# Optimization experiments

Measured on AMD Instinct MI355X. Metric: run time of the kernel, lower is better.

## Reference

```python
import jax, jax.numpy as jnp
import numpy as np

N = 100000
E = 1600000
IN_DIM = 128
OUT_DIM = 128


def setup_inputs() -> dict:
    key = jax.random.key(0)
    k1, k2, k3, k4 = jax.random.split(key, 4)
    x = jax.random.normal(k1, (N, IN_DIM), dtype=jnp.float32)
    edge_index = jax.random.randint(k2, (2, E), 0, N, dtype=jnp.int64)
    # GCNConv linear weight [in, out] and bias [out]
    W = jax.random.normal(k3, (IN_DIM, OUT_DIM), dtype=jnp.float32) / np.sqrt(IN_DIM)
    b = jax.random.normal(k4, (OUT_DIM,), dtype=jnp.float32) * 0.01
    return {"x": x, "edge_index": edge_index, "W": W, "b": b}


def reference(x, edge_index, W, b):
    n = x.shape[0]
    # linear transform first (PyG GCNConv applies lin before propagate)
    h = x @ W  # [N, OUT_DIM]
    # add self-loops
    loops = jnp.arange(n, dtype=edge_index.dtype)
    src = jnp.concatenate([edge_index[0], loops])
    dst = jnp.concatenate([edge_index[1], loops])
    # symmetric degree normalization (degree counted on dst, incl. self-loops)
    deg = jnp.zeros((n,), dtype=h.dtype).at[dst].add(1.0)
    dinv = jnp.where(deg > 0, jax.lax.rsqrt(deg), 0.0)
    norm = dinv[src] * dinv[dst]  # [E+N]
    # gather, scale, scatter-sum
    msgs = h[src] * norm[:, None]  # [E+N, OUT_DIM]
    out = jax.ops.segment_sum(msgs, dst, num_segments=n) + b
    return jax.nn.relu(out)
```

## Files before the change

### kernel.cpp

```cpp
#include <hip/hip_runtime.h>
#include <cstdint>
#include <cstddef>

#define IN_DIM 128
#define OUT_DIM 128
#define NR 8
#define ACAP 448
#define NS 256
#define NSUB_MAX 64
#define LCAP 192
#define SBCAP 4864
#define SCAP 4864

typedef int vint4 __attribute__((ext_vector_type(4)));
typedef float vfloat2 __attribute__((ext_vector_type(2)));
typedef short bf16x8 __attribute__((ext_vector_type(8)));
typedef float f32x4 __attribute__((ext_vector_type(4)));

__device__ __forceinline__ unsigned short f2bf(float f) {
  unsigned int u = __float_as_uint(f);
  u = (u + 0x7FFFu + ((u >> 16) & 1u)) >> 16;
  return (unsigned short)u;
}
__device__ __forceinline__ float bf_lo(unsigned int v) { return __uint_as_float(v << 16); }
__device__ __forceinline__ float bf_hi(unsigned int v) { return __uint_as_float(v & 0xFFFF0000u); }

__global__ void k_zero_i32(int* __restrict__ p, int n) {
  int i = blockIdx.x * blockDim.x + threadIdx.x;
  int st = gridDim.x * blockDim.x;
  for (; i < n; i += st) p[i] = 0;
}

__global__ void k_zero_f32(float* __restrict__ p, long long n) {
  long long i = (long long)blockIdx.x * blockDim.x + threadIdx.x;
  long long st = (long long)gridDim.x * blockDim.x;
  for (; i < n; i += st) p[i] = 0.0f;
}

__global__ void k_init(int* __restrict__ bmeta, int* __restrict__ sbcnt, int nB,
                       const float* __restrict__ W, unsigned short* __restrict__ Wt_g) {
  int gid = blockIdx.x * blockDim.x + threadIdx.x;
  int st = gridDim.x * blockDim.x;
  if (blockIdx.x == 0 && threadIdx.x < 16) bmeta[threadIdx.x] = 0;
  for (int i = gid; i < nB; i += st) sbcnt[i] = 0;
  for (int i = gid; i < IN_DIM * OUT_DIM; i += st) {
    int k = i >> 7, c = i & 127;
    Wt_g[c * IN_DIM + k] = f2bf(W[i]);
  }
}

__global__ void k_hist(const int* __restrict__ dst, int E, int* __restrict__ deg) {
  int i = blockIdx.x * blockDim.x + threadIdx.x;
  int st = gridDim.x * blockDim.x;
  for (; i < E; i += st) atomicAdd(&deg[dst[i]], 1);
}

__global__ void k_dinv(const int* __restrict__ deg, float* __restrict__ dinv, int n) {
  int i = blockIdx.x * blockDim.x + threadIdx.x;
  int st = gridDim.x * blockDim.x;
  for (; i < n; i += st) dinv[i] = rsqrtf((float)(deg[i] + 1));
}

__global__ __launch_bounds__(256) void k_bucket2(const int* __restrict__ ei, int E, int n,
                                                 unsigned int* __restrict__ bkt, int bcap,
                                                 int* __restrict__ bcnt,
                                                 int2* __restrict__ ovf, int* __restrict__ ocnt) {
  __shared__ unsigned int buf[NR][ACAP];
  __shared__ int cnt[NR];
  __shared__ int base[NR];
  const int rs = (n + NR - 1) / NR;
  const int tid = threadIdx.x;
  const int E4 = E >> 2;
  const vint4* s4 = (const vint4*)ei;
  const vint4* d4 = (const vint4*)(ei + E);
  const int nChunks = (E4 + 511) >> 9;

  for (int c = blockIdx.x; c < nChunks; c += gridDim.x) {
    if (tid < NR) cnt[tid] = 0;
    __syncthreads();
    const int i0 = c << 9;
#pragma unroll
    for (int u = 0; u < 2; ++u) {
      int i = i0 + (u << 8) + tid;
      if (i < E4) {
        vint4 s = __builtin_nontemporal_load(&s4[i]);
        vint4 d = __builtin_nontemporal_load(&d4[i]);
#define PUT(dd, ss)                                                                         \
        {                                                                                   \
          int rr = (dd) / rs;                                                               \
          unsigned int w = ((unsigned int)((dd) - rr * rs) << 17) | (unsigned int)(ss);     \
          int pos = atomicAdd(&cnt[rr], 1);                                                 \
          if (pos < ACAP) buf[rr][pos] = w;                                                 \
          else { int op = atomicAdd(ocnt, 1); ovf[op] = make_int2((ss), (dd)); }            \
        }
        PUT(d.x, s.x) PUT(d.y, s.y) PUT(d.z, s.z) PUT(d.w, s.w)
#undef PUT
      }
    }
    __syncthreads();
    if (tid < NR) {
      int m = cnt[tid]; if (m > ACAP) m = ACAP;
      base[tid] = atomicAdd(&bcnt[tid], m);
    }
    __syncthreads();
#pragma unroll
    for (int r = 0; r < NR; ++r) {
      int m = cnt[r]; if (m > ACAP) m = ACAP;
      int b = base[r];
      unsigned int* dp = bkt + (size_t)r * bcap;
      for (int j = tid; j < m; j += 256) {
        int idx = b + j;
        if (idx < bcap) __builtin_nontemporal_store(buf[r][j], &dp[idx]);
        else {
          unsigned int w = buf[r][j];
          int op = atomicAdd(ocnt, 1);
          ovf[op] = make_int2((int)(w & 0x1FFFFu), r * rs + (int)(w >> 17));
        }
      }
    }
    __syncthreads();
  }
  if (blockIdx.x == 0 && tid == 0) {
    for (int i = E4 << 2; i < E; ++i) {
      int s = ei[i], d = ei[E + i];
      int r = d / rs;
      int p = atomicAdd(&bcnt[r], 1);
      if (p < bcap) bkt[(size_t)r * bcap + p] = ((unsigned int)(d - r * rs) << 17) | (unsigned int)s;
      else { int op = atomicAdd(ocnt, 1); ovf[op] = make_int2(s, d); }
    }
  }
}

__global__ __launch_bounds__(256) void k_subbkt(const unsigned int* __restrict__ bkt, int bcap,
                                                const int* __restrict__ bcnt,
                                                unsigned int* __restrict__ sbkt,
                                                int* __restrict__ sbcnt, int nsub, int n,
                                                int2* __restrict__ ovf, int* __restrict__ ocnt) {
  __shared__ unsigned int buf[NSUB_MAX][LCAP];
  __shared__ int cnt[NSUB_MAX];
  __shared__ int base[NSUB_MAX];
  const int tid = threadIdx.x;
  const int r = blockIdx.x & 7;
  const int gblk = blockIdx.x >> 3;
  const int nblk = gridDim.x >> 3;
  const int rs = (n + NR - 1) / NR;
  int cr = bcnt[r]; if (cr > bcap) cr = bcap;
  const unsigned int* bp = bkt + (size_t)r * bcap;
  const int nChunks = (cr + 4095) >> 12;

  for (int c = gblk; c < nChunks; c += nblk) {
    for (int t = tid; t < nsub; t += 256) cnt[t] = 0;
    __syncthreads();
    const int i0 = c << 12;
    const int iend = min(i0 + 4096, cr);
    for (int i = i0 + tid; i < iend; i += 256) {
      unsigned int w = bp[i];
      int sub = (int)(w >> 25);
      int pos = atomicAdd(&cnt[sub], 1);
      if (pos < LCAP) buf[sub][pos] = w;
      else { int op = atomicAdd(ocnt, 1); ovf[op] = make_int2((int)(w & 0x1FFFFu), r * rs + (int)(w >> 17)); }
    }
    __syncthreads();
    for (int t = tid; t < nsub; t += 256) {
      int m = cnt[t]; if (m > LCAP) m = LCAP;
      base[t] = atomicAdd(&sbcnt[t * NR + r], m);
    }
    __syncthreads();
    for (int s = 0; s < nsub; ++s) {
      int m = cnt[s]; if (m > LCAP) m = LCAP;
      int b = base[s];
      unsigned int* dp = sbkt + (size_t)(s * NR + r) * SBCAP;
      for (int j = tid; j < m; j += 256) {
        int idx = b + j;
        if (idx < SBCAP) dp[idx] = buf[s][j];
        else {
          unsigned int w = buf[s][j];
          int op = atomicAdd(ocnt, 1);
          ovf[op] = make_int2((int)(w & 0x1FFFFu), r * rs + (int)(w >> 17));
        }
      }
    }
    __syncthreads();
  }
}

__global__ __launch_bounds__(256) void k_subsort2(const unsigned int* __restrict__ sbkt,
                                                  const int* __restrict__ sbcnt, int n,
                                                  int* __restrict__ csr, int* __restrict__ rs_start,
                                                  int* __restrict__ cur_end, float* __restrict__ dinv) {
  __shared__ unsigned int raw[SBCAP];
  __shared__ unsigned int srt[SBCAP];
  __shared__ int hist[NS];
  __shared__ int pref[NS];
  __shared__ int off[NS];
  const int tid = threadIdx.x;
  const int r = blockIdx.x & 7;
  const int sub = blockIdx.x >> 3;
  const int rs = (n + NR - 1) / NR;
  const int rsz = min(rs, n - r * rs);
  const int lo_dl = sub << 8;
  if (lo_dl >= rsz) return;
  const int nsn = min(NS, rsz - lo_dl);

  hist[tid] = 0;
  __syncthreads();

  int m = sbcnt[blockIdx.x]; if (m > SBCAP) m = SBCAP;
  const unsigned int* bp = sbkt + (size_t)blockIdx.x * SBCAP;
  for (int i = tid; i < m; i += 256) {
    unsigned int w = bp[i];
    raw[i] = w;
    atomicAdd(&hist[(int)(w >> 17) & (NS - 1)], 1);
  }
  __syncthreads();

  pref[tid] = hist[tid];
  __syncthreads();
  for (int o = 1; o < NS; o <<= 1) {
    int v = pref[tid] + ((tid >= o) ? pref[tid - o] : 0);
    __syncthreads();
    pref[tid] = v;
    __syncthreads();
  }
  off[tid] = pref[tid] - hist[tid];
  __syncthreads();

  for (int i = tid; i < m; i += 256) {
    unsigned int w = raw[i];
    int p = atomicAdd(&off[(int)(w >> 17) & (NS - 1)], 1);
    srt[p] = w & 0x1FFFFu;
  }
  __syncthreads();

  const int sbase = blockIdx.x * SCAP;
  for (int i = tid; i < m; i += 256) csr[sbase + i] = (int)srt[i];
  if (tid < nsn) {
    int node = r * rs + lo_dl + tid;
    rs_start[node] = sbase + pref[tid] - hist[tid];
    cur_end[node] = sbase + pref[tid];
    dinv[node] = rsqrtf((float)(hist[tid] + 1));
  }
}

__global__ void k_scatter_ovf(const int2* __restrict__ ovf, const int* __restrict__ ocnt,
                              int* __restrict__ cur_end, int* __restrict__ csr, int csr_total) {
  int m = *ocnt;
  for (int i = blockIdx.x * blockDim.x + threadIdx.x; i < m; i += gridDim.x * blockDim.x) {
    int2 e = ovf[i];
    int p = atomicAdd(&cur_end[e.y], 1);
    if (p >= 0 && p < csr_total) csr[p] = e.x;
  }
}

__global__ __launch_bounds__(256) void k_gemm_mfma(const float* __restrict__ x,
                                                   const unsigned short* __restrict__ Wt_g,
                                                   const float* __restrict__ dinv,
                                                   unsigned short* __restrict__ gb, int M) {
  __shared__ unsigned short xT[64][136];
  __shared__ unsigned short Wt[128][136];
  const int tid = threadIdx.x;
  const int row0 = blockIdx.x * 64;

  for (int i = tid; i < (IN_DIM * OUT_DIM) / 8; i += 256) {
    int c = i >> 4, k8 = (i & 15) * 8;
    uint4 v = *(const uint4*)(Wt_g + (size_t)c * IN_DIM + k8);
    *(uint4*)&Wt[c][k8] = v;
  }
  for (int i = tid; i < (64 * IN_DIM) / 4; i += 256) {
    int idx = i * 4;
    int r = idx >> 7, k = idx & 127;
    int grow = row0 + r; if (grow >= M) grow = M - 1;
    float4 v = *(const float4*)(x + (size_t)grow * IN_DIM + k);
    ushort4 b;
    b.x = f2bf(v.x); b.y = f2bf(v.y); b.z = f2bf(v.z); b.w = f2bf(v.w);
    *(ushort4*)&xT[r][k] = b;
  }
  __syncthreads();

  const int wv = tid >> 6;
  const int lane = tid & 63;
  const int l15 = lane & 15;
  const int lk8 = (lane >> 4) * 8;

  f32x4 acc[8];
#pragma unroll
  for (int ct = 0; ct < 8; ++ct) acc[ct] = (f32x4){0.f, 0.f, 0.f, 0.f};

#pragma unroll
  for (int kt = 0; kt < 4; ++kt) {
    bf16x8 a = *(const bf16x8*)&xT[wv * 16 + l15][kt * 32 + lk8];
#pragma unroll
    for (int ct = 0; ct < 8; ++ct) {
      bf16x8 b = *(const bf16x8*)&Wt[ct * 16 + l15][kt * 32 + lk8];
      acc[ct] = __builtin_amdgcn_mfma_f32_16x16x32_bf16(a, b, acc[ct], 0, 0, 0);
    }
  }

  const int drow0 = wv * 16 + (lane >> 4) * 4;
#pragma unroll
  for (int reg = 0; reg < 4; ++reg) {
    int grow = row0 + drow0 + reg;
    if (grow < M) {
      float s = dinv[grow];
      unsigned short* gp = gb + (size_t)grow * OUT_DIM + l15;
#pragma unroll
      for (int ct = 0; ct < 8; ++ct) {
        gp[ct * 16] = f2bf(acc[ct][reg] * s);
      }
    }
  }
}

__global__ __launch_bounds__(256) void k_gemm_scale(const float* __restrict__ x, const float* __restrict__ W,
                                                    const float* __restrict__ dinv,
                                                    unsigned short* __restrict__ gb, int M) {
  __shared__ float xT[32][128];
  __shared__ float Ws[32][128];
  const int tid = threadIdx.x;
  const int tc = tid & 15;
  const int tr = tid >> 4;
  const int row0 = blockIdx.x * 128;
  const int lr = tid & 127;
  const int lk = (tid >> 7) * 16;

  float acc[8][8] = {};

  for (int k0 = 0; k0 < IN_DIM; k0 += 32) {
    int grow = row0 + lr;
    if (grow >= M) grow = M - 1;
    const float4* xp = (const float4*)(x + (size_t)grow * IN_DIM + k0 + lk);
    float4 a0 = xp[0], a1 = xp[1], a2 = xp[2], a3 = xp[3];
    const float4* wp = (const float4*)(W + (size_t)(k0 + (tid >> 3)) * OUT_DIM + (tid & 7) * 16);
    float4 w0 = wp[0], w1 = wp[1], w2 = wp[2], w3 = wp[3];

    __syncthreads();
    xT[lk + 0][lr] = a0.x;  xT[lk + 1][lr] = a0.y;  xT[lk + 2][lr] = a0.z;  xT[lk + 3][lr] = a0.w;
    xT[lk + 4][lr] = a1.x;  xT[lk + 5][lr] = a1.y;  xT[lk + 6][lr] = a1.z;  xT[lk + 7][lr] = a1.w;
    xT[lk + 8][lr] = a2.x;  xT[lk + 9][lr] = a2.y;  xT[lk + 10][lr] = a2.z; xT[lk + 11][lr] = a2.w;
    xT[lk + 12][lr] = a3.x; xT[lk + 13][lr] = a3.y; xT[lk + 14][lr] = a3.z; xT[lk + 15][lr] = a3.w;
    float4* wsp = (float4*)&Ws[tid >> 3][(tid & 7) * 16];
    wsp[0] = w0; wsp[1] = w1; wsp[2] = w2; wsp[3] = w3;
    __syncthreads();

#pragma unroll
    for (int k = 0; k < 32; ++k) {
      float xv[8], wvv[8];
      *(float4*)&xv[0] = *(const float4*)&xT[k][tr * 8];
      *(float4*)&xv[4] = *(const float4*)&xT[k][tr * 8 + 4];
      *(float4*)&wvv[0] = *(const float4*)&Ws[k][tc * 8];
      *(float4*)&wvv[4] = *(const float4*)&Ws[k][tc * 8 + 4];
#pragma unroll
      for (int ii = 0; ii < 8; ++ii)
#pragma unroll
        for (int jj = 0; jj < 8; ++jj)
          acc[ii][jj] = fmaf(xv[ii], wvv[jj], acc[ii][jj]);
    }
  }

#pragma unroll
  for (int ii = 0; ii < 8; ++ii) {
    int rr = row0 + tr * 8 + ii;
    if (rr < M) {
      float s = dinv[rr];
      uint4 o;
      o.x = (unsigned int)f2bf(acc[ii][0] * s) | ((unsigned int)f2bf(acc[ii][1] * s) << 16);
      o.y = (unsigned int)f2bf(acc[ii][2] * s) | ((unsigned int)f2bf(acc[ii][3] * s) << 16);
      o.z = (unsigned int)f2bf(acc[ii][4] * s) | ((unsigned int)f2bf(acc[ii][5] * s) << 16);
      o.w = (unsigned int)f2bf(acc[ii][6] * s) | ((unsigned int)f2bf(acc[ii][7] * s) << 16);
      *(uint4*)(gb + (size_t)rr * OUT_DIM + tc * 8) = o;
    }
  }
}

__global__ __launch_bounds__(256) void k_agg_se(const unsigned short* __restrict__ gb,
                                                const int* __restrict__ rs_start, const int* __restrict__ cur_end,
                                                const int* __restrict__ csr, const float* __restrict__ dinv,
                                                const float* __restrict__ bias, float* __restrict__ out, int n) {
  const int lane = threadIdx.x & 63;
  const int wave = __builtin_amdgcn_readfirstlane(threadIdx.x >> 6);
  const int wpb = blockDim.x >> 6;
  const int nWaves = gridDim.x * wpb;
  const int c2 = lane * 2;
  const float2 bb = *(const float2*)(bias + c2);

  for (int node = blockIdx.x * wpb + wave; node < n; node += nWaves) {
    const int s = rs_start[node];
    const int e = cur_end[node];
    unsigned int sv = *(const unsigned int*)(gb + (size_t)node * OUT_DIM + c2);
    float ax = bf_lo(sv), ay = bf_hi(sv);
    int i = s;
    for (; i + 8 <= e; i += 8) {
      int s0 = csr[i + 0], s1 = csr[i + 1], s2 = csr[i + 2], s3 = csr[i + 3];
      int s4 = csr[i + 4], s5 = csr[i + 5], s6 = csr[i + 6], s7 = csr[i + 7];
      unsigned int v0 = *(const unsigned int*)(gb + (size_t)s0 * OUT_DIM + c2);
      unsigned int v1 = *(const unsigned int*)(gb + (size_t)s1 * OUT_DIM + c2);
      unsigned int v2 = *(const unsigned int*)(gb + (size_t)s2 * OUT_DIM + c2);
      unsigned int v3 = *(const unsigned int*)(gb + (size_t)s3 * OUT_DIM + c2);
      unsigned int v4 = *(const unsigned int*)(gb + (size_t)s4 * OUT_DIM + c2);
      unsigned int v5 = *(const unsigned int*)(gb + (size_t)s5 * OUT_DIM + c2);
      unsigned int v6 = *(const unsigned int*)(gb + (size_t)s6 * OUT_DIM + c2);
      unsigned int v7 = *(const unsigned int*)(gb + (size_t)s7 * OUT_DIM + c2);
      ax += ((bf_lo(v0) + bf_lo(v1)) + (bf_lo(v2) + bf_lo(v3))) +
            ((bf_lo(v4) + bf_lo(v5)) + (bf_lo(v6) + bf_lo(v7)));
      ay += ((bf_hi(v0) + bf_hi(v1)) + (bf_hi(v2) + bf_hi(v3))) +
            ((bf_hi(v4) + bf_hi(v5)) + (bf_hi(v6) + bf_hi(v7)));
    }
    for (; i < e; ++i) {
      unsigned int v = *(const unsigned int*)(gb + (size_t)csr[i] * OUT_DIM + c2);
      ax += bf_lo(v);
      ay += bf_hi(v);
    }
    const float di = dinv[node];
    vfloat2 o;
    o.x = fmaxf(fmaf(ax, di, bb.x), 0.0f);
    o.y = fmaxf(fmaf(ay, di, bb.y), 0.0f);
    __builtin_nontemporal_store(o, (vfloat2*)(out + (size_t)node * OUT_DIM + c2));
  }
}

__global__ __launch_bounds__(256) void k_scatter(const int* __restrict__ ei, int E,
                                                 const unsigned short* __restrict__ gb, float* __restrict__ out) {
  const int lane = threadIdx.x & 63;
  const int wave = __builtin_amdgcn_readfirstlane(threadIdx.x >> 6);
  const int wpb = blockDim.x >> 6;
  const int nWaves = gridDim.x * wpb;
  const int c2 = lane * 2;
  for (int e = blockIdx.x * wpb + wave; e < E; e += nWaves) {
    int s = ei[e];
    int d = ei[E + e];
    unsigned int v = *(const unsigned int*)(gb + (size_t)s * OUT_DIM + c2);
    atomicAdd(&out[(size_t)d * OUT_DIM + c2 + 0], bf_lo(v));
    atomicAdd(&out[(size_t)d * OUT_DIM + c2 + 1], bf_hi(v));
  }
}

__global__ void k_finalize(const unsigned short* __restrict__ gb, const float* __restrict__ dinv,
                           const float* __restrict__ bias, float* __restrict__ out, int n) {
  int i = blockIdx.x * blockDim.x + threadIdx.x;
  int st = gridDim.x * blockDim.x;
  int total = n * OUT_DIM;
  for (; i < total; i += st) {
    int node = i >> 7;
    float gv = __uint_as_float(((unsigned int)gb[i]) << 16);
    float v = (out[i] + gv) * dinv[node] + bias[i & 127];
    out[i] = fmaxf(v, 0.0f);
  }
}

extern "C" void kernel_launch(void* const* d_in, const int* in_sizes, int n_in,
                              void* d_out, int out_size, void* d_ws, size_t ws_size,
                              hipStream_t stream) {
  const float* x = (const float*)d_in[0];
  const int* ei = (const int*)d_in[1];
  const float* W = (const float*)d_in[2];
  const float* bias = (const float*)d_in[3];
  float* out = (float*)d_out;

  const int N = in_sizes[0] / IN_DIM;
  const int E = in_sizes[1] / 2;

  const int rs = (N + NR - 1) / NR;
  const int nsub = (rs + NS - 1) / NS;
  const int nBlocksB = nsub * NR;
  const int csr_total = nBlocksB * SCAP;
  const int bcap = E / NR + E / 64 + 256;
  const int mBlocks64 = (N + 63) / 64;

  char* ws = (char*)d_ws;
  size_t off = 0;
  auto alloc = [&](size_t bytes) -> void* {
    void* p = ws + off;
    off += (bytes + 255) & ~(size_t)255;
    return p;
  };

  unsigned short* gb = (unsigned short*)alloc((size_t)N * OUT_DIM * sizeof(unsigned short));
  float* dinv = (float*)alloc((size_t)N * sizeof(float));
  int* rs_start = (int*)alloc((size_t)N * sizeof(int));
  int* cur_end = (int*)alloc((size_t)N * sizeof(int));
  int* csr = (int*)alloc((size_t)csr_total * sizeof(int));
  unsigned int* bkt = (unsigned int*)alloc((size_t)NR * bcap * sizeof(unsigned int));
  unsigned int* sbkt = (unsigned int*)alloc((size_t)nBlocksB * SBCAP * sizeof(unsigned int));
  int* sbcnt = (int*)alloc((size_t)nBlocksB * sizeof(int));
  unsigned short* Wt_g = (unsigned short*)alloc((size_t)IN_DIM * OUT_DIM * sizeof(unsigned short));
  int* bmeta = (int*)alloc(16 * sizeof(int));
  int2* ovf = (int2*)alloc((size_t)(E / 8 + 1024) * sizeof(int2));
  size_t bucket_need = off;

  const bool bucketed = (ws_size >= bucket_need) && (N <= (1 << 17)) && (rs <= (1 << 14)) &&
                        (nsub <= NSUB_MAX);

  if (bucketed) {
    k_init<<<64, 256, 0, stream>>>(bmeta, sbcnt, nBlocksB, W, Wt_g);
    int aGrid = ((E >> 2) + 511) >> 9;
    if (aGrid < 1) aGrid = 1;
    k_bucket2<<<aGrid, 256, 0, stream>>>(ei, E, N, bkt, bcap, bmeta, ovf, bmeta + 8);
    k_subbkt<<<nBlocksB, 256, 0, stream>>>(bkt, bcap, bmeta, sbkt, sbcnt, nsub, N, ovf, bmeta + 8);
    k_subsort2<<<nBlocksB, 256, 0, stream>>>(sbkt, sbcnt, N, csr, rs_start, cur_end, dinv);
    k_gemm_mfma<<<mBlocks64, 256, 0, stream>>>(x, Wt_g, dinv, gb, N);
    k_scatter_ovf<<<64, 256, 0, stream>>>(ovf, bmeta + 8, cur_end, csr, csr_total);
    k_agg_se<<<2048, 256, 0, stream>>>(gb, rs_start, cur_end, csr, dinv, bias, out, N);
  } else {
    off = 0;
    unsigned short* gb2 = (unsigned short*)alloc((size_t)N * OUT_DIM * sizeof(unsigned short));
    int* deg = (int*)alloc((size_t)N * sizeof(int));
    float* dinv2 = (float*)alloc((size_t)N * sizeof(float));
    if (ws_size < off) return;
    k_zero_i32<<<256, 256, 0, stream>>>(deg, N);
    k_hist<<<2048, 256, 0, stream>>>(ei + E, E, deg);
    k_dinv<<<512, 256, 0, stream>>>(deg, dinv2, N);
    k_gemm_scale<<<(N + 127) / 128, 256, 0, stream>>>(x, W, dinv2, gb2, N);
    k_zero_f32<<<2048, 256, 0, stream>>>(out, (long long)N * OUT_DIM);
    k_scatter<<<4096, 256, 0, stream>>>(ei, E, gb2, out);
    k_finalize<<<2048, 256, 0, stream>>>(gb2, dinv2, bias, out, N);
  }
}
```

Measured before the change: 152.7 us.

## Split aggregation into two column-half passes to shrink gather working set

```diff
diff --git a/kernel.cpp b/kernel.cpp
--- a/kernel.cpp
+++ b/kernel.cpp
@@ -24,6 +24,7 @@
 }
 __device__ __forceinline__ float bf_lo(unsigned int v) { return __uint_as_float(v << 16); }
 __device__ __forceinline__ float bf_hi(unsigned int v) { return __uint_as_float(v & 0xFFFF0000u); }
+__device__ __forceinline__ float bf1(unsigned short v) { return __uint_as_float(((unsigned int)v) << 16); }
 
 __global__ void k_zero_i32(int* __restrict__ p, int n) {
   int i = blockIdx.x * blockDim.x + threadIdx.x;
@@ -372,49 +373,41 @@
   }
 }
 
-__global__ __launch_bounds__(256) void k_agg_se(const unsigned short* __restrict__ gb,
-                                                const int* __restrict__ rs_start, const int* __restrict__ cur_end,
-                                                const int* __restrict__ csr, const float* __restrict__ dinv,
-                                                const float* __restrict__ bias, float* __restrict__ out, int n) {
+__global__ __launch_bounds__(256) void k_agg_half(const unsigned short* __restrict__ gb,
+                                                  const int* __restrict__ rs_start, const int* __restrict__ cur_end,
+                                                  const int* __restrict__ csr, const float* __restrict__ dinv,
+                                                  const float* __restrict__ bias, float* __restrict__ out,
+                                                  int n, int half) {
   const int lane = threadIdx.x & 63;
   const int wave = __builtin_amdgcn_readfirstlane(threadIdx.x >> 6);
   const int wpb = blockDim.x >> 6;
   const int nWaves = gridDim.x * wpb;
-  const int c2 = lane * 2;
-  const float2 bb = *(const float2*)(bias + c2);
+  const int col = half * 64 + lane;
+  const float bb = bias[col];
 
   for (int node = blockIdx.x * wpb + wave; node < n; node += nWaves) {
     const int s = rs_start[node];
     const int e = cur_end[node];
-    unsigned int sv = *(const unsigned int*)(gb + (size_t)node * OUT_DIM + c2);
-    float ax = bf_lo(sv), ay = bf_hi(sv);
+    float ax = bf1(gb[(size_t)node * OUT_DIM + col]);
     int i = s;
     for (; i + 8 <= e; i += 8) {
       int s0 = csr[i + 0], s1 = csr[i + 1], s2 = csr[i + 2], s3 = csr[i + 3];
       int s4 = csr[i + 4], s5 = csr[i + 5], s6 = csr[i + 6], s7 = csr[i + 7];
-      unsigned int v0 = *(const unsigned int*)(gb + (size_t)s0 * OUT_DIM + c2);
-      unsigned int v1 = *(const unsigned int*)(gb + (size_t)s1 * OUT_DIM + c2);
-      unsigned int v2 = *(const unsigned int*)(gb + (size_t)s2 * OUT_DIM + c2);
-      unsigned int v3 = *(const unsigned int*)(gb + (size_t)s3 * OUT_DIM + c2);
-      unsigned int v4 = *(const unsigned int*)(gb + (size_t)s4 * OUT_DIM + c2);
-      unsigned int v5 = *(const unsigned int*)(gb + (size_t)s5 * OUT_DIM + c2);
-      unsigned int v6 = *(const unsigned int*)(gb + (size_t)s6 * OUT_DIM + c2);
-      unsigned int v7 = *(const unsigned int*)(gb + (size_t)s7 * OUT_DIM + c2);
-      ax += ((bf_lo(v0) + bf_lo(v1)) + (bf_lo(v2) + bf_lo(v3))) +
-            ((bf_lo(v4) + bf_lo(v5)) + (bf_lo(v6) + bf_lo(v7)));
-      ay += ((bf_hi(v0) + bf_hi(v1)) + (bf_hi(v2) + bf_hi(v3))) +
-            ((bf_hi(v4) + bf_hi(v5)) + (bf_hi(v6) + bf_hi(v7)));
+      float v0 = bf1(gb[(size_t)s0 * OUT_DIM + col]);
+      float v1 = bf1(gb[(size_t)s1 * OUT_DIM + col]);
+      float v2 = bf1(gb[(size_t)s2 * OUT_DIM + col]);
+      float v3 = bf1(gb[(size_t)s3 * OUT_DIM + col]);
+      float v4 = bf1(gb[(size_t)s4 * OUT_DIM + col]);
+      float v5 = bf1(gb[(size_t)s5 * OUT_DIM + col]);
+      float v6 = bf1(gb[(size_t)s6 * OUT_DIM + col]);
+      float v7 = bf1(gb[(size_t)s7 * OUT_DIM + col]);
+      ax += ((v0 + v1) + (v2 + v3)) + ((v4 + v5) + (v6 + v7));
     }
     for (; i < e; ++i) {
-      unsigned int v = *(const unsigned int*)(gb + (size_t)csr[i] * OUT_DIM + c2);
-      ax += bf_lo(v);
-      ay += bf_hi(v);
-    }
-    const float di = dinv[node];
-    vfloat2 o;
-    o.x = fmaxf(fmaf(ax, di, bb.x), 0.0f);
-    o.y = fmaxf(fmaf(ay, di, bb.y), 0.0f);
-    __builtin_nontemporal_store(o, (vfloat2*)(out + (size_t)node * OUT_DIM + c2));
+      ax += bf1(gb[(size_t)csr[i] * OUT_DIM + col]);
+    }
+    float o = fmaxf(fmaf(ax, dinv[node], bb), 0.0f);
+    __builtin_nontemporal_store(o, out + (size_t)node * OUT_DIM + col);
   }
 }
 
@@ -499,7 +492,8 @@
     k_subsort2<<<nBlocksB, 256, 0, stream>>>(sbkt, sbcnt, N, csr, rs_start, cur_end, dinv);
     k_gemm_mfma<<<mBlocks64, 256, 0, stream>>>(x, Wt_g, dinv, gb, N);
     k_scatter_ovf<<<64, 256, 0, stream>>>(ovf, bmeta + 8, cur_end, csr, csr_total);
-    k_agg_se<<<2048, 256, 0, stream>>>(gb, rs_start, cur_end, csr, dinv, bias, out, N);
+    k_agg_half<<<2048, 256, 0, stream>>>(gb, rs_start, cur_end, csr, dinv, bias, out, N, 0);
+    k_agg_half<<<2048, 256, 0, stream>>>(gb, rs_start, cur_end, csr, dinv, bias, out, N, 1);
   } else {
     off = 0;
     unsigned short* gb2 = (unsigned short*)alloc((size_t)N * OUT_DIM * sizeof(unsigned short));
```

After: 176.6 us. +15.6%, slower.

## Fuse two-level edge bucketing into a single direct sub-bucket pass

Applied to the files above, without the earlier changes.

```diff
diff --git a/kernel.cpp b/kernel.cpp
--- a/kernel.cpp
+++ b/kernel.cpp
@@ -5,10 +5,9 @@
 #define IN_DIM 128
 #define OUT_DIM 128
 #define NR 8
-#define ACAP 448
 #define NS 256
 #define NSUB_MAX 64
-#define LCAP 192
+#define LCAP 128
 #define SBCAP 4864
 #define SCAP 4864
 
@@ -61,81 +60,10 @@
   for (; i < n; i += st) dinv[i] = rsqrtf((float)(deg[i] + 1));
 }
 
-__global__ __launch_bounds__(256) void k_bucket2(const int* __restrict__ ei, int E, int n,
-                                                 unsigned int* __restrict__ bkt, int bcap,
-                                                 int* __restrict__ bcnt,
-                                                 int2* __restrict__ ovf, int* __restrict__ ocnt) {
-  __shared__ unsigned int buf[NR][ACAP];
-  __shared__ int cnt[NR];
-  __shared__ int base[NR];
-  const int rs = (n + NR - 1) / NR;
-  const int tid = threadIdx.x;
-  const int E4 = E >> 2;
-  const vint4* s4 = (const vint4*)ei;
-  const vint4* d4 = (const vint4*)(ei + E);
-  const int nChunks = (E4 + 511) >> 9;
-
-  for (int c = blockIdx.x; c < nChunks; c += gridDim.x) {
-    if (tid < NR) cnt[tid] = 0;
-    __syncthreads();
-    const int i0 = c << 9;
-#pragma unroll
-    for (int u = 0; u < 2; ++u) {
-      int i = i0 + (u << 8) + tid;
-      if (i < E4) {
-        vint4 s = __builtin_nontemporal_load(&s4[i]);
-        vint4 d = __builtin_nontemporal_load(&d4[i]);
-#define PUT(dd, ss)                                                                         \
-        {                                                                                   \
-          int rr = (dd) / rs;                                                               \
-          unsigned int w = ((unsigned int)((dd) - rr * rs) << 17) | (unsigned int)(ss);     \
-          int pos = atomicAdd(&cnt[rr], 1);                                                 \
-          if (pos < ACAP) buf[rr][pos] = w;                                                 \
-          else { int op = atomicAdd(ocnt, 1); ovf[op] = make_int2((ss), (dd)); }            \
-        }
-        PUT(d.x, s.x) PUT(d.y, s.y) PUT(d.z, s.z) PUT(d.w, s.w)
-#undef PUT
-      }
-    }
-    __syncthreads();
-    if (tid < NR) {
-      int m = cnt[tid]; if (m > ACAP) m = ACAP;
-      base[tid] = atomicAdd(&bcnt[tid], m);
-    }
-    __syncthreads();
-#pragma unroll
-    for (int r = 0; r < NR; ++r) {
-      int m = cnt[r]; if (m > ACAP) m = ACAP;
-      int b = base[r];
-      unsigned int* dp = bkt + (size_t)r * bcap;
-      for (int j = tid; j < m; j += 256) {
-        int idx = b + j;
-        if (idx < bcap) __builtin_nontemporal_store(buf[r][j], &dp[idx]);
-        else {
-          unsigned int w = buf[r][j];
-          int op = atomicAdd(ocnt, 1);
-          ovf[op] = make_int2((int)(w & 0x1FFFFu), r * rs + (int)(w >> 17));
-        }
-      }
-    }
-    __syncthreads();
-  }
-  if (blockIdx.x == 0 && tid == 0) {
-    for (int i = E4 << 2; i < E; ++i) {
-      int s = ei[i], d = ei[E + i];
-      int r = d / rs;
-      int p = atomicAdd(&bcnt[r], 1);
-      if (p < bcap) bkt[(size_t)r * bcap + p] = ((unsigned int)(d - r * rs) << 17) | (unsigned int)s;
-      else { int op = atomicAdd(ocnt, 1); ovf[op] = make_int2(s, d); }
-    }
-  }
-}
-
-__global__ __launch_bounds__(256) void k_subbkt(const unsigned int* __restrict__ bkt, int bcap,
-                                                const int* __restrict__ bcnt,
-                                                unsigned int* __restrict__ sbkt,
-                                                int* __restrict__ sbcnt, int nsub, int n,
-                                                int2* __restrict__ ovf, int* __restrict__ ocnt) {
+__global__ __launch_bounds__(256) void k_bucket_direct(const int* __restrict__ ei, int E, int n,
+                                                       unsigned int* __restrict__ sbkt,
+                                                       int* __restrict__ sbcnt, int nsub,
+                                                       int2* __restrict__ ovf, int* __restrict__ ocnt) {
   __shared__ unsigned int buf[NSUB_MAX][LCAP];
   __shared__ int cnt[NSUB_MAX];
   __shared__ int base[NSUB_MAX];
@@ -144,39 +72,57 @@
   const int gblk = blockIdx.x >> 3;
   const int nblk = gridDim.x >> 3;
   const int rs = (n + NR - 1) / NR;
-  int cr = bcnt[r]; if (cr > bcap) cr = bcap;
-  const unsigned int* bp = bkt + (size_t)r * bcap;
-  const int nChunks = (cr + 4095) >> 12;
+  const int lo = r * rs;
+  const int hi = (lo + rs < n) ? lo + rs : n;
+  const int E4 = E >> 2;
+  const vint4* s4 = (const vint4*)ei;
+  const vint4* d4 = (const vint4*)(ei + E);
+  int nChunks = (E4 + 1023) >> 10;
+  if (nChunks == 0) nChunks = 1;
 
   for (int c = gblk; c < nChunks; c += nblk) {
     for (int t = tid; t < nsub; t += 256) cnt[t] = 0;
     __syncthreads();
-    const int i0 = c << 12;
-    const int iend = min(i0 + 4096, cr);
+    const int i0 = c << 10;
+    const int iend = min(i0 + 1024, E4);
+#define PUT(dd, ss)                                                                          \
+    if ((dd) >= lo && (dd) < hi) {                                                           \
+      int dl = (dd) - lo;                                                                    \
+      int sb = dl >> 8;                                                                      \
+      int pos = atomicAdd(&cnt[sb], 1);                                                      \
+      if (pos < LCAP) buf[sb][pos] = ((unsigned int)dl << 17) | (unsigned int)(ss);          \
+      else { int op = atomicAdd(ocnt, 1); ovf[op] = make_int2((ss), (dd)); }                 \
+    }
     for (int i = i0 + tid; i < iend; i += 256) {
-      unsigned int w = bp[i];
-      int sub = (int)(w >> 25);
-      int pos = atomicAdd(&cnt[sub], 1);
-      if (pos < LCAP) buf[sub][pos] = w;
-      else { int op = atomicAdd(ocnt, 1); ovf[op] = make_int2((int)(w & 0x1FFFFu), r * rs + (int)(w >> 17)); }
-    }
+      vint4 s = __builtin_nontemporal_load(&s4[i]);
+      vint4 d = __builtin_nontemporal_load(&d4[i]);
+      PUT(d.x, s.x) PUT(d.y, s.y) PUT(d.z, s.z) PUT(d.w, s.w)
+    }
+    if (iend == E4) {
+      for (int j = (E4 << 2) + tid; j < E; j += 256) {
+        int ss = ei[j];
+        int dd = ei[E + j];
+        PUT(dd, ss)
+      }
+    }
+#undef PUT
     __syncthreads();
     for (int t = tid; t < nsub; t += 256) {
       int m = cnt[t]; if (m > LCAP) m = LCAP;
-      base[t] = atomicAdd(&sbcnt[t * NR + r], m);
-    }
-    __syncthreads();
-    for (int s = 0; s < nsub; ++s) {
-      int m = cnt[s]; if (m > LCAP) m = LCAP;
-      int b = base[s];
-      unsigned int* dp = sbkt + (size_t)(s * NR + r) * SBCAP;
+      base[t] = m ? atomicAdd(&sbcnt[t * NR + r], m) : 0;
+    }
+    __syncthreads();
+    for (int s2 = 0; s2 < nsub; ++s2) {
+      int m = cnt[s2]; if (m > LCAP) m = LCAP;
+      int b = base[s2];
+      unsigned int* dp = sbkt + (size_t)(s2 * NR + r) * SBCAP;
       for (int j = tid; j < m; j += 256) {
         int idx = b + j;
-        if (idx < SBCAP) dp[idx] = buf[s][j];
+        if (idx < SBCAP) __builtin_nontemporal_store(buf[s2][j], &dp[idx]);
         else {
-          unsigned int w = buf[s][j];
+          unsigned int w = buf[s2][j];
           int op = atomicAdd(ocnt, 1);
-          ovf[op] = make_int2((int)(w & 0x1FFFFu), r * rs + (int)(w >> 17));
+          ovf[op] = make_int2((int)(w & 0x1FFFFu), lo + (int)(w >> 17));
         }
       }
     }
@@ -463,7 +409,6 @@
   const int nsub = (rs + NS - 1) / NS;
   const int nBlocksB = nsub * NR;
   const int csr_total = nBlocksB * SCAP;
-  const int bcap = E / NR + E / 64 + 256;
   const int mBlocks64 = (N + 63) / 64;
 
   char* ws = (char*)d_ws;
@@ -479,7 +424,6 @@
   int* rs_start = (int*)alloc((size_t)N * sizeof(int));
   int* cur_end = (int*)alloc((size_t)N * sizeof(int));
   int* csr = (int*)alloc((size_t)csr_total * sizeof(int));
-  unsigned int* bkt = (unsigned int*)alloc((size_t)NR * bcap * sizeof(unsigned int));
   unsigned int* sbkt = (unsigned int*)alloc((size_t)nBlocksB * SBCAP * sizeof(unsigned int));
   int* sbcnt = (int*)alloc((size_t)nBlocksB * sizeof(int));
   unsigned short* Wt_g = (unsigned short*)alloc((size_t)IN_DIM * OUT_DIM * sizeof(unsigned short));
@@ -488,14 +432,11 @@
   size_t bucket_need = off;
 
   const bool bucketed = (ws_size >= bucket_need) && (N <= (1 << 17)) && (rs <= (1 << 14)) &&
-                        (nsub <= NSUB_MAX);
+                        (nsub <= NSUB_MAX) && ((E & 3) == 0 || E < 4);
 
   if (bucketed) {
     k_init<<<64, 256, 0, stream>>>(bmeta, sbcnt, nBlocksB, W, Wt_g);
-    int aGrid = ((E >> 2) + 511) >> 9;
-    if (aGrid < 1) aGrid = 1;
-    k_bucket2<<<aGrid, 256, 0, stream>>>(ei, E, N, bkt, bcap, bmeta, ovf, bmeta + 8);
-    k_subbkt<<<nBlocksB, 256, 0, stream>>>(bkt, bcap, bmeta, sbkt, sbcnt, nsub, N, ovf, bmeta + 8);
+    k_bucket_direct<<<2048, 256, 0, stream>>>(ei, E, N, sbkt, sbcnt, nsub, ovf, bmeta + 8);
     k_subsort2<<<nBlocksB, 256, 0, stream>>>(sbkt, sbcnt, N, csr, rs_start, cur_end, dinv);
     k_gemm_mfma<<<mBlocks64, 256, 0, stream>>>(x, Wt_g, dinv, gb, N);
     k_scatter_ovf<<<64, 256, 0, stream>>>(ovf, bmeta + 8, cur_end, csr, csr_total);
```

Result: slower. 190.9 us (+25.1%).
